# Kernel optimization log

Measured on AMD Instinct MI355X. Metric: run time of the kernel, lower is better.

Reference implementation:

```python
import jax, jax.numpy as jnp
import numpy as np

B, C, F, TP = 16, 64, 128, 100
E = 576
NFEAT, NHID, NOUT = 128, 128, 64
RATIO = 0.9
BN_EPS = 1e-5


def setup_inputs() -> dict:
    key = jax.random.key(0)
    ks = jax.random.split(key, 16)
    s = 0.05
    h = jax.random.normal(ks[0], (B, C, F, TP), jnp.float32)
    edge_index = jax.random.randint(ks[1], (2, E), 0, C, dtype=jnp.int32)
    edge_weight = jax.random.uniform(ks[2], (E,), jnp.float32)
    W1 = jax.random.normal(ks[3], (NFEAT, NHID), jnp.float32) / np.float32(np.sqrt(NFEAT))
    b1 = s * jax.random.normal(ks[4], (NHID,), jnp.float32)
    g1 = 1.0 + s * jax.random.normal(ks[5], (NHID,), jnp.float32)
    be1 = s * jax.random.normal(ks[6], (NHID,), jnp.float32)
    a1 = jnp.full((1,), 0.25, jnp.float32)  # PReLU slope
    Wp = jax.random.normal(ks[7], (NHID, 1), jnp.float32) / np.float32(np.sqrt(NHID))
    bp = s * jax.random.normal(ks[8], (1,), jnp.float32)
    W2 = jax.random.normal(ks[9], (NHID, NOUT), jnp.float32) / np.float32(np.sqrt(NHID))
    b2 = s * jax.random.normal(ks[10], (NOUT,), jnp.float32)
    g2 = 1.0 + s * jax.random.normal(ks[11], (NOUT,), jnp.float32)
    be2 = s * jax.random.normal(ks[12], (NOUT,), jnp.float32)
    a2 = jnp.full((1,), 0.25, jnp.float32)
    return dict(h=h, edge_index=edge_index, edge_weight=edge_weight,
                W1=W1, b1=b1, g1=g1, be1=be1, a1=a1, Wp=Wp, bp=bp,
                W2=W2, b2=b2, g2=g2, be2=be2, a2=a2)


def gcn_conv(x, W, b, row, col, ew, N):
    # PyG GCNConv: add self-loops (weight 1), symmetric normalization, x@W, scatter-add to col.
    si = jnp.arange(N, dtype=row.dtype)
    r = jnp.concatenate([row, si])
    c = jnp.concatenate([col, si])
    w = jnp.concatenate([ew, jnp.ones((N,), x.dtype)])
    deg = jax.ops.segment_sum(w, c, num_segments=N)
    dis = jnp.where(deg > 0, jax.lax.rsqrt(jnp.maximum(deg, 1e-12)), 0.0)
    norm = dis[r] * w * dis[c]
    hlin = x @ W
    out = jax.ops.segment_sum(hlin[r] * norm[:, None], c, num_segments=N)
    return out + b


def batchnorm(x, g, beta):
    m = jnp.mean(x, axis=0)
    v = jnp.mean((x - m) ** 2, axis=0)  # biased var, as in torch BN training
    return (x - m) * jax.lax.rsqrt(v + BN_EPS) * g + beta


def prelu(x, a):
    return jnp.where(x >= 0, x, a * x)


def reference(h, edge_index, edge_weight, W1, b1, g1, be1, a1, Wp, bp, W2, b2, g2, be2, a2):
    Bv, Cv, Fv, Tpv = h.shape
    G = Bv * Tpv                      # num_graphs
    N = G * Cv                        # total nodes
    K = int(np.ceil(RATIO * Cv))      # kept nodes per graph (static)
    x = jnp.transpose(h, (0, 3, 1, 2)).reshape(N, Fv)
    Ev = edge_index.shape[1]
    offs = jnp.repeat(jnp.arange(G, dtype=edge_index.dtype) * Cv, Ev)
    row = jnp.tile(edge_index[0], G) + offs
    col = jnp.tile(edge_index[1], G) + offs
    ew = jnp.tile(edge_weight, G)
    # gc1 -> bn1 -> prelu
    x = prelu(batchnorm(gcn_conv(x, W1, b1, row, col, ew, N), g1, be1), a1)
    # SAGPooling: score GNN (GCNConv, no edge weights), tanh, per-graph top-k
    score = jnp.tanh(gcn_conv(x, Wp, bp, row, col, jnp.ones_like(ew), N)[:, 0])
    topv, topi = jax.lax.top_k(score.reshape(G, Cv), K)
    perm = (topi + (jnp.arange(G, dtype=topi.dtype) * Cv)[:, None]).reshape(-1)
    xk = x[perm] * topv.reshape(-1)[:, None]
    Nk = G * K
    new_id = jnp.zeros((N,), jnp.int32).at[perm].set(jnp.arange(Nk, dtype=jnp.int32))
    kept = jnp.zeros((N,), bool).at[perm].set(True)
    valid = kept[row] & kept[col]
    r2 = new_id[row]
    c2 = new_id[col]
    w2 = jnp.where(valid, ew, 0.0)    # dropped edges: weight 0 == filtered out
    # gc2 -> bn2 -> prelu (dropout is identity in eval)
    x2 = prelu(batchnorm(gcn_conv(xk, W2, b2, r2, c2, w2, Nk), g2, be2), a2)
    # global mean pool: exactly K nodes per graph, contiguous
    z = x2.reshape(G, K, -1).mean(axis=1)
    z_seq = jnp.transpose(z.reshape(Bv, Tpv, -1), (0, 2, 1))
    return x2, z_seq
```

## Files before the change

### kernel.cpp

```cpp
#include <hip/hip_runtime.h>

constexpr int Bc   = 16;
constexpr int Cc   = 64;
constexpr int Fc   = 128;
constexpr int TPc  = 100;
constexpr int Gc   = Bc * TPc;
constexpr int Nc   = Gc * Cc;
constexpr int Ec   = 576;
constexpr int NHID = 128;
constexpr int NOUTc= 64;
constexpr int Kc   = 58;
constexpr int Nkc  = Gc * Kc;

__global__ void k0_prep(const int* __restrict__ ei, const float* __restrict__ ew,
                        float* __restrict__ A1, float* __restrict__ AP,
                        double* bn1S, double* bn1Q, double* bn2S, double* bn2Q) {
    __shared__ float deg1[64], degP[64], dis1[64], disP[64];
    __shared__ float A1L[4096], APL[4096];
    int t = threadIdx.x;
    if (t < 64) { deg1[t] = 1.0f; degP[t] = 1.0f; }
    for (int i = t; i < 4096; i += 256) { A1L[i] = 0.f; APL[i] = 0.f; }
    if (t < 128) { bn1S[t] = 0.0; bn1Q[t] = 0.0; }
    if (t < 64)  { bn2S[t] = 0.0; bn2Q[t] = 0.0; }
    __syncthreads();
    for (int e = t; e < Ec; e += 256) {
        int c = ei[Ec + e];
        atomicAdd(&deg1[c], ew[e]);
        atomicAdd(&degP[c], 1.0f);
    }
    __syncthreads();
    if (t < 64) { dis1[t] = 1.0f / sqrtf(deg1[t]); disP[t] = 1.0f / sqrtf(degP[t]); }
    __syncthreads();
    for (int e = t; e < Ec; e += 256) {
        int r = ei[e], c = ei[Ec + e];
        atomicAdd(&A1L[c * 64 + r], dis1[r] * ew[e] * dis1[c]);
        atomicAdd(&APL[c * 64 + r], disP[r] * disP[c]);
    }
    __syncthreads();
    if (t < 64) {
        A1L[t * 65] += dis1[t] * dis1[t];
        APL[t * 65] += disP[t] * disP[t];
    }
    __syncthreads();
    for (int i = t; i < 4096; i += 256) { A1[i] = A1L[i]; AP[i] = APL[i]; }
}

__global__ __launch_bounds__(256)
void k_trans(const float* __restrict__ h, float* __restrict__ XT) {
    __shared__ float tile[64 * 101];
    int blk = blockIdx.x;
    int b = blk >> 7, f = blk & 127;
    int t = threadIdx.x;
    const float* hb = h + (size_t)b * 819200 + (size_t)f * 100;
    for (int i = t; i < 6400; i += 256) {
        unsigned c = (unsigned)i / 100u;
        unsigned tp = (unsigned)i - c * 100u;
        tile[c * 101 + tp] = hb[(size_t)c * 12800 + tp];
    }
    __syncthreads();
    float* xb = XT + (size_t)b * 100 * 8192 + f * 64;
    for (int j = t; j < 6400; j += 256) {
        int tp = j >> 6, c = j & 63;
        xb[(size_t)tp * 8192 + c] = tile[c * 101 + tp];
    }
}

__global__ __launch_bounds__(256, 4)
void k1_gc1(const float* __restrict__ XT, const float* __restrict__ W1,
            const float* __restrict__ b1, const float* __restrict__ A1,
            float* __restrict__ Y1, double* bn1S, double* bn1Q) {
    __shared__ float S[8192];
    int g = blockIdx.x;
    int t = threadIdx.x;
    int tx = t & 31, ty = t >> 5;

    const float4* wsrc = (const float4*)W1;
    const float4* xsrc = (const float4*)(XT + (size_t)g * 8192);

    float4 w0 = wsrc[t], w1 = wsrc[256 + t], w2 = wsrc[512 + t], w3 = wsrc[768 + t];
    float4 xp0 = xsrc[t], xp1 = xsrc[256 + t];

    float acc[8][4];
#pragma unroll
    for (int i = 0; i < 8; ++i)
#pragma unroll
        for (int j = 0; j < 4; ++j) acc[i][j] = 0.f;

    for (int kq = 0; kq < 4; ++kq) {
        {
            float4* wdst = (float4*)S;
            wdst[t]       = w0;
            wdst[256 + t] = w1;
            wdst[512 + t] = w2;
            wdst[768 + t] = w3;
            float4* xdst = (float4*)(S + 4096);
            xdst[t]       = xp0;
            xdst[256 + t] = xp1;
        }
        if (kq < 3) {
            const float4* wn = wsrc + (kq + 1) * 1024;
            const float4* xn = xsrc + (kq + 1) * 512;
            w0 = wn[t]; w1 = wn[256 + t]; w2 = wn[512 + t]; w3 = wn[768 + t];
            xp0 = xn[t]; xp1 = xn[256 + t];
        }
        __syncthreads();
        for (int kk = 0; kk < 32; ++kk) {
            float4 xa = *(const float4*)&S[4096 + kk * 64 + ty * 8];
            float4 xb = *(const float4*)&S[4096 + kk * 64 + ty * 8 + 4];
            float4 w  = *(const float4*)&S[kk * 128 + tx * 4];
            float xr[8] = {xa.x, xa.y, xa.z, xa.w, xb.x, xb.y, xb.z, xb.w};
#pragma unroll
            for (int i = 0; i < 8; ++i) {
                acc[i][0] += xr[i] * w.x;
                acc[i][1] += xr[i] * w.y;
                acc[i][2] += xr[i] * w.z;
                acc[i][3] += xr[i] * w.w;
            }
        }
        __syncthreads();
    }
#pragma unroll
    for (int i = 0; i < 8; ++i) {
        float4 v = make_float4(acc[i][0], acc[i][1], acc[i][2], acc[i][3]);
        *(float4*)&S[(ty * 8 + i) * 128 + tx * 4] = v;
    }
    __syncthreads();
    float acy[8][4];
    float4 bb = *(const float4*)&b1[tx * 4];
#pragma unroll
    for (int i = 0; i < 8; ++i) { acy[i][0] = bb.x; acy[i][1] = bb.y; acy[i][2] = bb.z; acy[i][3] = bb.w; }
    for (int rr = 0; rr < 16; ++rr) {
        float4 hrow[4];
#pragma unroll
        for (int q = 0; q < 4; ++q) hrow[q] = *(const float4*)&S[(rr * 4 + q) * 128 + tx * 4];
#pragma unroll
        for (int i = 0; i < 8; ++i) {
            float4 a4 = *(const float4*)&A1[(ty * 8 + i) * 64 + rr * 4];
            acy[i][0] += a4.x * hrow[0].x + a4.y * hrow[1].x + a4.z * hrow[2].x + a4.w * hrow[3].x;
            acy[i][1] += a4.x * hrow[0].y + a4.y * hrow[1].y + a4.z * hrow[2].y + a4.w * hrow[3].y;
            acy[i][2] += a4.x * hrow[0].z + a4.y * hrow[1].z + a4.z * hrow[2].z + a4.w * hrow[3].z;
            acy[i][3] += a4.x * hrow[0].w + a4.y * hrow[1].w + a4.z * hrow[2].w + a4.w * hrow[3].w;
        }
    }
    float ps[4] = {0, 0, 0, 0}, pq[4] = {0, 0, 0, 0};
    float* Yg = Y1 + (size_t)g * 64 * 128;
#pragma unroll
    for (int i = 0; i < 8; ++i) {
        float4 v = make_float4(acy[i][0], acy[i][1], acy[i][2], acy[i][3]);
        *(float4*)&Yg[(ty * 8 + i) * 128 + tx * 4] = v;
#pragma unroll
        for (int j = 0; j < 4; ++j) { ps[j] += acy[i][j]; pq[j] += acy[i][j] * acy[i][j]; }
    }
    __syncthreads();
    float* redS = S;
    float* redQ = S + 1024;
#pragma unroll
    for (int j = 0; j < 4; ++j) {
        redS[ty * 128 + tx * 4 + j] = ps[j];
        redQ[ty * 128 + tx * 4 + j] = pq[j];
    }
    __syncthreads();
    if (t < 128) {
        float Sv = 0.f, Q = 0.f;
        for (int y = 0; y < 8; ++y) { Sv += redS[y * 128 + t]; Q += redQ[y * 128 + t]; }
        atomicAdd(&bn1S[t], (double)Sv);
        atomicAdd(&bn1Q[t], (double)Q);
    }
}

__global__ void k_bnfin(const double* __restrict__ S, const double* __restrict__ Q,
                        const float* __restrict__ gam, const float* __restrict__ bet,
                        float* __restrict__ scale, float* __restrict__ shift, double invN) {
    int t = threadIdx.x;
    double m = S[t] * invN;
    double v = Q[t] * invN - m * m;
    double rstd = 1.0 / sqrt(v + 1e-5);
    float sc = (float)((double)gam[t] * rstd);
    scale[t] = sc;
    shift[t] = bet[t] - (float)m * sc;
}

__global__ __launch_bounds__(256, 2)
void k3a_pool(float* __restrict__ Y1, const float* __restrict__ scale1,
              const float* __restrict__ shift1, const float* __restrict__ a1,
              const float* __restrict__ Wp, const float* __restrict__ bp,
              const float* __restrict__ AP, const float* __restrict__ W2) {
    __shared__ float Xs[64 * 132];
    __shared__ float slin[64], psum[256], score[64];
    __shared__ int   rnk[64], ord[64];
    int g = blockIdx.x, t = threadIdx.x;
    int tx = t & 31, ty = t >> 5;
    float alpha1 = a1[0];

    float* slab = Y1 + (size_t)g * 8192;
    {
        const float4* Yg4 = (const float4*)slab;
        float4 sc4 = *(const float4*)&scale1[tx * 4];
        float4 sh4 = *(const float4*)&shift1[tx * 4];
#pragma unroll
        for (int it = 0; it < 8; ++it) {
            int e4 = it * 256 + t;
            int c = e4 >> 5;
            float4 v = Yg4[e4];
            v.x = v.x * sc4.x + sh4.x; v.x = (v.x >= 0.f) ? v.x : alpha1 * v.x;
            v.y = v.y * sc4.y + sh4.y; v.y = (v.y >= 0.f) ? v.y : alpha1 * v.y;
            v.z = v.z * sc4.z + sh4.z; v.z = (v.z >= 0.f) ? v.z : alpha1 * v.z;
            v.w = v.w * sc4.w + sh4.w; v.w = (v.w >= 0.f) ? v.w : alpha1 * v.w;
            *(float4*)&Xs[c * 132 + tx * 4] = v;
        }
    }
    __syncthreads();
    {
        int rr = t >> 2, q4 = t & 3;
        float sp = 0.f;
        for (int m = 0; m < 32; ++m) sp += Xs[rr * 132 + q4 * 32 + m] * Wp[q4 * 32 + m];
        psum[t] = sp;
    }
    __syncthreads();
    if (t < 64) slin[t] = psum[t * 4] + psum[t * 4 + 1] + psum[t * 4 + 2] + psum[t * 4 + 3];
    __syncthreads();
    if (t < 64) {
        float acc = bp[0];
        for (int r = 0; r < 64; ++r) acc += AP[t * 64 + r] * slin[r];
        score[t] = tanhf(acc);
    }
    __syncthreads();
    if (t < 64) {
        float sc = score[t];
        int cnt = 0;
        for (int c2 = 0; c2 < 64; ++c2) {
            float o = score[c2];
            cnt += (o > sc) || (o == sc && c2 < t);
        }
        rnk[t] = cnt;
        if (cnt < Kc) ord[cnt] = t;
        ((int*)(slab + 4096))[t] = cnt;
    }
    __syncthreads();

    {
        int row0 = ty * 8;
        float acc2[8][2];
        int   cidx[8];
        float srow[8];
#pragma unroll
        for (int i = 0; i < 8; ++i) {
            acc2[i][0] = 0.f; acc2[i][1] = 0.f;
            int r = row0 + i;
            if (r < Kc) { cidx[i] = ord[r]; srow[i] = score[cidx[i]]; }
            else        { cidx[i] = 0;      srow[i] = 0.f; }
        }
        for (int k0 = 0; k0 < 128; k0 += 4) {
            float4 xv[8];
#pragma unroll
            for (int i = 0; i < 8; ++i) xv[i] = *(const float4*)&Xs[cidx[i] * 132 + k0];
#pragma unroll
            for (int q = 0; q < 4; ++q) {
                float2 w = *(const float2*)&W2[(k0 + q) * 64 + tx * 2];
#pragma unroll
                for (int i = 0; i < 8; ++i) {
                    float xq = (q == 0) ? xv[i].x : (q == 1) ? xv[i].y : (q == 2) ? xv[i].z : xv[i].w;
                    acc2[i][0] += xq * w.x;
                    acc2[i][1] += xq * w.y;
                }
            }
        }
#pragma unroll
        for (int i = 0; i < 8; ++i) {
            *(float2*)&slab[(row0 + i) * 64 + tx * 2] =
                make_float2(acc2[i][0] * srow[i], acc2[i][1] * srow[i]);
        }
    }
}

__global__ __launch_bounds__(256, 2)
void k3b_gc2(const float* __restrict__ Y1, const int* __restrict__ ei,
             const float* __restrict__ ew, const float* __restrict__ b2,
             float* __restrict__ Y2, double* bn2S, double* bn2Q) {
    __shared__ float H2s[64 * 68];
    __shared__ float A2s[4096];
    __shared__ float dis2[64], deg2[64];
    __shared__ int   rnk[64];
    int g = blockIdx.x, t = threadIdx.x;
    int tx = t & 31, ty = t >> 5;

    const float* slab = Y1 + (size_t)g * 8192;
    {
        const float4* src = (const float4*)slab;
#pragma unroll
        for (int it = 0; it < 4; ++it) {
            int i4 = it * 256 + t;
            int r = i4 >> 4, c4 = i4 & 15;
            *(float4*)&H2s[r * 68 + c4 * 4] = src[i4];
        }
    }
    if (t < 64) rnk[t] = ((const int*)(slab + 4096))[t];
    {
        float4 z = make_float4(0.f, 0.f, 0.f, 0.f);
        float4* A2s4 = (float4*)A2s;
#pragma unroll
        for (int j = 0; j < 4; ++j) A2s4[j * 256 + t] = z;
    }
    if (t < 64) deg2[t] = 1.0f;
    __syncthreads();
    for (int e = t; e < Ec; e += 256) {
        int r = ei[e], c = ei[Ec + e];
        if (rnk[r] < Kc && rnk[c] < Kc) atomicAdd(&deg2[rnk[c]], ew[e]);
    }
    __syncthreads();
    if (t < 64) dis2[t] = 1.0f / sqrtf(deg2[t]);
    __syncthreads();
    for (int e = t; e < Ec; e += 256) {
        int r = ei[e], c = ei[Ec + e];
        int rkr = rnk[r], rkc = rnk[c];
        if (rkr < Kc && rkc < Kc) atomicAdd(&A2s[rkc * 64 + rkr], dis2[rkr] * ew[e] * dis2[rkc]);
    }
    __syncthreads();
    if (t < Kc) A2s[t * 65] += dis2[t] * dis2[t];
    __syncthreads();

    float acy[8][2];
    float2 b2v = *(const float2*)&b2[tx * 2];
#pragma unroll
    for (int i = 0; i < 8; ++i) { acy[i][0] = b2v.x; acy[i][1] = b2v.y; }
    for (int rr = 0; rr < 16; ++rr) {
        float2 h2[4];
#pragma unroll
        for (int q = 0; q < 4; ++q) h2[q] = *(const float2*)&H2s[(rr * 4 + q) * 68 + tx * 2];
#pragma unroll
        for (int i = 0; i < 8; ++i) {
            float4 a4 = *(const float4*)&A2s[(ty * 8 + i) * 64 + rr * 4];
            acy[i][0] += a4.x * h2[0].x + a4.y * h2[1].x + a4.z * h2[2].x + a4.w * h2[3].x;
            acy[i][1] += a4.x * h2[0].y + a4.y * h2[1].y + a4.z * h2[2].y + a4.w * h2[3].y;
        }
    }
    float s0 = 0.f, s1 = 0.f, q0 = 0.f, q1 = 0.f;
    float* Y2g = Y2 + (size_t)g * Kc * 64;
#pragma unroll
    for (int i = 0; i < 8; ++i) {
        int ck = ty * 8 + i;
        if (ck < Kc) {
            float2 v = make_float2(acy[i][0], acy[i][1]);
            *(float2*)&Y2g[ck * 64 + tx * 2] = v;
            s0 += v.x; s1 += v.y; q0 += v.x * v.x; q1 += v.y * v.y;
        }
    }
    __syncthreads();
    float* redS = H2s;
    float* redQ = H2s + 512;
    redS[ty * 64 + tx * 2]     = s0;
    redS[ty * 64 + tx * 2 + 1] = s1;
    redQ[ty * 64 + tx * 2]     = q0;
    redQ[ty * 64 + tx * 2 + 1] = q1;
    __syncthreads();
    if (t < 64) {
        float S = 0.f, Q = 0.f;
        for (int y = 0; y < 8; ++y) { S += redS[y * 64 + t]; Q += redQ[y * 64 + t]; }
        atomicAdd(&bn2S[t], (double)S);
        atomicAdd(&bn2Q[t], (double)Q);
    }
}

__global__ void k5_out(const float* __restrict__ Y2, const float* __restrict__ scale2,
                       const float* __restrict__ shift2, const float* __restrict__ a2v,
                       float* __restrict__ out) {
    __shared__ float red[4 * 64];
    int g = blockIdx.x, t = threadIdx.x;
    float alpha = a2v[0];
    const float* Yg = Y2 + (size_t)g * Kc * 64;
    float* Og = out + (size_t)g * Kc * 64;
    int c = t & 63, rg = t >> 6;
    float part = 0.f;
    for (int rk = rg; rk < Kc; rk += 4) {
        float v = Yg[rk * 64 + c] * scale2[c] + shift2[c];
        v = (v >= 0.f) ? v : alpha * v;
        Og[rk * 64 + c] = v;
        part += v;
    }
    red[rg * 64 + c] = part;
    __syncthreads();
    if (t < 64) {
        float z = (red[t] + red[64 + t] + red[128 + t] + red[192 + t]) / (float)Kc;
        int b = g / TPc, tp = g % TPc;
        out[(size_t)Nkc * 64 + (size_t)b * NOUTc * TPc + t * TPc + tp] = z;
    }
}

extern "C" void kernel_launch(void* const* d_in, const int* in_sizes, int n_in,
                              void* d_out, int out_size, void* d_ws, size_t ws_size,
                              hipStream_t stream) {
    const float* h   = (const float*)d_in[0];
    const int*   ei  = (const int*)  d_in[1];
    const float* ew  = (const float*)d_in[2];
    const float* W1  = (const float*)d_in[3];
    const float* b1  = (const float*)d_in[4];
    const float* g1  = (const float*)d_in[5];
    const float* be1 = (const float*)d_in[6];
    const float* a1  = (const float*)d_in[7];
    const float* Wp  = (const float*)d_in[8];
    const float* bp  = (const float*)d_in[9];
    const float* W2  = (const float*)d_in[10];
    const float* b2  = (const float*)d_in[11];
    const float* g2  = (const float*)d_in[12];
    const float* be2 = (const float*)d_in[13];
    const float* a2  = (const float*)d_in[14];

    char* ws = (char*)d_ws;
    double* bn1S   = (double*)(ws + 0);
    double* bn1Q   = (double*)(ws + 1024);
    double* bn2S   = (double*)(ws + 2048);
    double* bn2Q   = (double*)(ws + 2560);
    float*  scale1 = (float*)(ws + 3072);
    float*  shift1 = (float*)(ws + 3584);
    float*  scale2 = (float*)(ws + 4096);
    float*  shift2 = (float*)(ws + 4352);
    float*  A1     = (float*)(ws + 4608);
    float*  AP     = (float*)(ws + 20992);
    float*  XT     = (float*)(ws + 37376);
    float*  Y1     = XT;
    float*  Y2     = (float*)(ws + 37376 + 52428800);
    float*  out    = (float*)d_out;

    hipLaunchKernelGGL(k0_prep, dim3(1), dim3(256), 0, stream,
                       ei, ew, A1, AP, bn1S, bn1Q, bn2S, bn2Q);
    hipLaunchKernelGGL(k_trans, dim3(2048), dim3(256), 0, stream, h, XT);
    hipLaunchKernelGGL(k1_gc1, dim3(Gc), dim3(256), 0, stream,
                       XT, W1, b1, A1, Y1, bn1S, bn1Q);
    hipLaunchKernelGGL(k_bnfin, dim3(1), dim3(128), 0, stream,
                       bn1S, bn1Q, g1, be1, scale1, shift1, 1.0 / (double)Nc);
    hipLaunchKernelGGL(k3a_pool, dim3(Gc), dim3(256), 0, stream,
                       Y1, scale1, shift1, a1, Wp, bp, AP, W2);
    hipLaunchKernelGGL(k3b_gc2, dim3(Gc), dim3(256), 0, stream,
                       Y1, ei, ew, b2, Y2, bn2S, bn2Q);
    hipLaunchKernelGGL(k_bnfin, dim3(1), dim3(64), 0, stream,
                       bn2S, bn2Q, g2, be2, scale2, shift2, 1.0 / (double)Nkc);
    hipLaunchKernelGGL(k5_out, dim3(Gc), dim3(256), 0, stream,
                       Y2, scale2, shift2, a2, out);
}
```

Before: 232.0 us.

## Process two graphs per block in gc1 to reuse W1 tiles

Each k1_gc1 block now handles two graphs, so every W1 tile loaded into shared memory serves two X tiles. This halves W1 global/shared traffic per graph and halves the number of BN atomic adds, but doubles the accumulator registers (64 floats) under launch_bounds(256,4). It also drops the register prefetch double-buffering and launches only 800 blocks, which lowers occupancy and latency hiding.

```diff
diff --git a/kernel.cpp b/kernel.cpp
--- a/kernel.cpp
+++ b/kernel.cpp
@@ -70,88 +70,128 @@
             const float* __restrict__ b1, const float* __restrict__ A1,
             float* __restrict__ Y1, double* bn1S, double* bn1Q) {
     __shared__ float S[8192];
-    int g = blockIdx.x;
+    int g0 = blockIdx.x * 2, g1 = g0 + 1;
     int t = threadIdx.x;
     int tx = t & 31, ty = t >> 5;
 
-    const float4* wsrc = (const float4*)W1;
-    const float4* xsrc = (const float4*)(XT + (size_t)g * 8192);
-
-    float4 w0 = wsrc[t], w1 = wsrc[256 + t], w2 = wsrc[512 + t], w3 = wsrc[768 + t];
-    float4 xp0 = xsrc[t], xp1 = xsrc[256 + t];
-
-    float acc[8][4];
+    const float4* x0src = (const float4*)(XT + (size_t)g0 * 8192);
+    const float4* x1src = (const float4*)(XT + (size_t)g1 * 8192);
+
+    float acc0[8][4], acc1[8][4];
 #pragma unroll
     for (int i = 0; i < 8; ++i)
 #pragma unroll
-        for (int j = 0; j < 4; ++j) acc[i][j] = 0.f;
+        for (int j = 0; j < 4; ++j) { acc0[i][j] = 0.f; acc1[i][j] = 0.f; }
 
     for (int kq = 0; kq < 4; ++kq) {
+        __syncthreads();
         {
-            float4* wdst = (float4*)S;
-            wdst[t]       = w0;
-            wdst[256 + t] = w1;
-            wdst[512 + t] = w2;
-            wdst[768 + t] = w3;
-            float4* xdst = (float4*)(S + 4096);
-            xdst[t]       = xp0;
-            xdst[256 + t] = xp1;
-        }
-        if (kq < 3) {
-            const float4* wn = wsrc + (kq + 1) * 1024;
-            const float4* xn = xsrc + (kq + 1) * 512;
-            w0 = wn[t]; w1 = wn[256 + t]; w2 = wn[512 + t]; w3 = wn[768 + t];
-            xp0 = xn[t]; xp1 = xn[256 + t];
+            float4* d0 = (float4*)S;
+            d0[t]       = x0src[kq * 512 + t];
+            d0[256 + t] = x0src[kq * 512 + 256 + t];
+            float4* d1 = (float4*)(S + 2048);
+            d1[t]       = x1src[kq * 512 + t];
+            d1[256 + t] = x1src[kq * 512 + 256 + t];
+            const float4* wsrc = (const float4*)(W1 + kq * 4096);
+            float4* wd = (float4*)(S + 4096);
+#pragma unroll
+            for (int it = 0; it < 4; ++it) wd[it * 256 + t] = wsrc[it * 256 + t];
         }
         __syncthreads();
         for (int kk = 0; kk < 32; ++kk) {
-            float4 xa = *(const float4*)&S[4096 + kk * 64 + ty * 8];
-            float4 xb = *(const float4*)&S[4096 + kk * 64 + ty * 8 + 4];
-            float4 w  = *(const float4*)&S[kk * 128 + tx * 4];
-            float xr[8] = {xa.x, xa.y, xa.z, xa.w, xb.x, xb.y, xb.z, xb.w};
+            float4 xa0 = *(const float4*)&S[kk * 64 + ty * 8];
+            float4 xb0 = *(const float4*)&S[kk * 64 + ty * 8 + 4];
+            float4 xa1 = *(const float4*)&S[2048 + kk * 64 + ty * 8];
+            float4 xb1 = *(const float4*)&S[2048 + kk * 64 + ty * 8 + 4];
+            float4 w   = *(const float4*)&S[4096 + kk * 128 + tx * 4];
+            float xr0[8] = {xa0.x, xa0.y, xa0.z, xa0.w, xb0.x, xb0.y, xb0.z, xb0.w};
+            float xr1[8] = {xa1.x, xa1.y, xa1.z, xa1.w, xb1.x, xb1.y, xb1.z, xb1.w};
 #pragma unroll
             for (int i = 0; i < 8; ++i) {
-                acc[i][0] += xr[i] * w.x;
-                acc[i][1] += xr[i] * w.y;
-                acc[i][2] += xr[i] * w.z;
-                acc[i][3] += xr[i] * w.w;
+                acc0[i][0] += xr0[i] * w.x;
+                acc0[i][1] += xr0[i] * w.y;
+                acc0[i][2] += xr0[i] * w.z;
+                acc0[i][3] += xr0[i] * w.w;
+                acc1[i][0] += xr1[i] * w.x;
+                acc1[i][1] += xr1[i] * w.y;
+                acc1[i][2] += xr1[i] * w.z;
+                acc1[i][3] += xr1[i] * w.w;
             }
         }
-        __syncthreads();
-    }
+    }
+    __syncthreads();
+
+    float ps[4] = {0, 0, 0, 0}, pq[4] = {0, 0, 0, 0};
+    float4 bb = *(const float4*)&b1[tx * 4];
+
 #pragma unroll
     for (int i = 0; i < 8; ++i) {
-        float4 v = make_float4(acc[i][0], acc[i][1], acc[i][2], acc[i][3]);
+        float4 v = make_float4(acc0[i][0], acc0[i][1], acc0[i][2], acc0[i][3]);
         *(float4*)&S[(ty * 8 + i) * 128 + tx * 4] = v;
     }
     __syncthreads();
-    float acy[8][4];
-    float4 bb = *(const float4*)&b1[tx * 4];
-#pragma unroll
-    for (int i = 0; i < 8; ++i) { acy[i][0] = bb.x; acy[i][1] = bb.y; acy[i][2] = bb.z; acy[i][3] = bb.w; }
-    for (int rr = 0; rr < 16; ++rr) {
-        float4 hrow[4];
-#pragma unroll
-        for (int q = 0; q < 4; ++q) hrow[q] = *(const float4*)&S[(rr * 4 + q) * 128 + tx * 4];
+    {
+        float acy[8][4];
+#pragma unroll
+        for (int i = 0; i < 8; ++i) { acy[i][0] = bb.x; acy[i][1] = bb.y; acy[i][2] = bb.z; acy[i][3] = bb.w; }
+        for (int rr = 0; rr < 16; ++rr) {
+            float4 hrow[4];
+#pragma unroll
+            for (int q = 0; q < 4; ++q) hrow[q] = *(const float4*)&S[(rr * 4 + q) * 128 + tx * 4];
+#pragma unroll
+            for (int i = 0; i < 8; ++i) {
+                float4 a4 = *(const float4*)&A1[(ty * 8 + i) * 64 + rr * 4];
+                acy[i][0] += a4.x * hrow[0].x + a4.y * hrow[1].x + a4.z * hrow[2].x + a4.w * hrow[3].x;
+                acy[i][1] += a4.x * hrow[0].y + a4.y * hrow[1].y + a4.z * hrow[2].y + a4.w * hrow[3].y;
+                acy[i][2] += a4.x * hrow[0].z + a4.y * hrow[1].z + a4.z * hrow[2].z + a4.w * hrow[3].z;
+                acy[i][3] += a4.x * hrow[0].w + a4.y * hrow[1].w + a4.z * hrow[2].w + a4.w * hrow[3].w;
+            }
+        }
+        float* Yg = Y1 + (size_t)g0 * 8192;
 #pragma unroll
         for (int i = 0; i < 8; ++i) {
-            float4 a4 = *(const float4*)&A1[(ty * 8 + i) * 64 + rr * 4];
-            acy[i][0] += a4.x * hrow[0].x + a4.y * hrow[1].x + a4.z * hrow[2].x + a4.w * hrow[3].x;
-            acy[i][1] += a4.x * hrow[0].y + a4.y * hrow[1].y + a4.z * hrow[2].y + a4.w * hrow[3].y;
-            acy[i][2] += a4.x * hrow[0].z + a4.y * hrow[1].z + a4.z * hrow[2].z + a4.w * hrow[3].z;
-            acy[i][3] += a4.x * hrow[0].w + a4.y * hrow[1].w + a4.z * hrow[2].w + a4.w * hrow[3].w;
-        }
-    }
-    float ps[4] = {0, 0, 0, 0}, pq[4] = {0, 0, 0, 0};
-    float* Yg = Y1 + (size_t)g * 64 * 128;
+            float4 v = make_float4(acy[i][0], acy[i][1], acy[i][2], acy[i][3]);
+            *(float4*)&Yg[(ty * 8 + i) * 128 + tx * 4] = v;
+#pragma unroll
+            for (int j = 0; j < 4; ++j) { ps[j] += acy[i][j]; pq[j] += acy[i][j] * acy[i][j]; }
+        }
+    }
+    __syncthreads();
+
 #pragma unroll
     for (int i = 0; i < 8; ++i) {
-        float4 v = make_float4(acy[i][0], acy[i][1], acy[i][2], acy[i][3]);
-        *(float4*)&Yg[(ty * 8 + i) * 128 + tx * 4] = v;
-#pragma unroll
-        for (int j = 0; j < 4; ++j) { ps[j] += acy[i][j]; pq[j] += acy[i][j] * acy[i][j]; }
-    }
-    __syncthreads();
+        float4 v = make_float4(acc1[i][0], acc1[i][1], acc1[i][2], acc1[i][3]);
+        *(float4*)&S[(ty * 8 + i) * 128 + tx * 4] = v;
+    }
+    __syncthreads();
+    {
+        float acy[8][4];
+#pragma unroll
+        for (int i = 0; i < 8; ++i) { acy[i][0] = bb.x; acy[i][1] = bb.y; acy[i][2] = bb.z; acy[i][3] = bb.w; }
+        for (int rr = 0; rr < 16; ++rr) {
+            float4 hrow[4];
+#pragma unroll
+            for (int q = 0; q < 4; ++q) hrow[q] = *(const float4*)&S[(rr * 4 + q) * 128 + tx * 4];
+#pragma unroll
+            for (int i = 0; i < 8; ++i) {
+                float4 a4 = *(const float4*)&A1[(ty * 8 + i) * 64 + rr * 4];
+                acy[i][0] += a4.x * hrow[0].x + a4.y * hrow[1].x + a4.z * hrow[2].x + a4.w * hrow[3].x;
+                acy[i][1] += a4.x * hrow[0].y + a4.y * hrow[1].y + a4.z * hrow[2].y + a4.w * hrow[3].y;
+                acy[i][2] += a4.x * hrow[0].z + a4.y * hrow[1].z + a4.z * hrow[2].z + a4.w * hrow[3].z;
+                acy[i][3] += a4.x * hrow[0].w + a4.y * hrow[1].w + a4.z * hrow[2].w + a4.w * hrow[3].w;
+            }
+        }
+        float* Yg = Y1 + (size_t)g1 * 8192;
+#pragma unroll
+        for (int i = 0; i < 8; ++i) {
+            float4 v = make_float4(acy[i][0], acy[i][1], acy[i][2], acy[i][3]);
+            *(float4*)&Yg[(ty * 8 + i) * 128 + tx * 4] = v;
+#pragma unroll
+            for (int j = 0; j < 4; ++j) { ps[j] += acy[i][j]; pq[j] += acy[i][j] * acy[i][j]; }
+        }
+    }
+    __syncthreads();
+
     float* redS = S;
     float* redQ = S + 1024;
 #pragma unroll
@@ -424,7 +464,7 @@
     hipLaunchKernelGGL(k0_prep, dim3(1), dim3(256), 0, stream,
                        ei, ew, A1, AP, bn1S, bn1Q, bn2S, bn2Q);
     hipLaunchKernelGGL(k_trans, dim3(2048), dim3(256), 0, stream, h, XT);
-    hipLaunchKernelGGL(k1_gc1, dim3(Gc), dim3(256), 0, stream,
+    hipLaunchKernelGGL(k1_gc1, dim3(Gc / 2), dim3(256), 0, stream,
                        XT, W1, b1, A1, Y1, bn1S, bn1Q);
     hipLaunchKernelGGL(k_bnfin, dim3(1), dim3(128), 0, stream,
                        bn1S, bn1Q, g1, be1, scale1, shift1, 1.0 / (double)Nc);
```

New measurement: 235.6 us. About the same (+1.5%).
